# Performance work log

Hardware: AMD Instinct MI355X
Metric: run time of the kernel (lower is better)

Reference implementation:

```python
import jax, jax.numpy as jnp
import numpy as np

DN = ('NCHW', 'OIHW', 'NCHW')
EPS = 1e-5


def _mask_time(x, lengths):
    # zero out positions t >= length along the last (time) axis
    T = x.shape[-1]
    valid = jnp.arange(T)[None, None, None, :] < lengths[:, None, None, None]
    return jnp.where(valid, x, jnp.zeros((), x.dtype))


def _conv(x, w, b, stride, pad):
    y = jax.lax.conv_general_dilated(x, w, window_strides=stride,
                                     padding=[(pad[0], pad[0]), (pad[1], pad[1])],
                                     dimension_numbers=DN)
    return y + b[None, :, None, None]


def _bn(x, g, be, m, v):
    inv = jax.lax.rsqrt(v + EPS)
    return (x - m[None, :, None, None]) * (g * inv)[None, :, None, None] + be[None, :, None, None]


def setup_inputs() -> dict:
    key = jax.random.key(0)
    ks = jax.random.split(key, 16)
    f32 = jnp.float32
    return {
        'x': jax.random.normal(ks[0], (16, 1, 161, 1024), f32),
        'x_lengths': jax.random.randint(ks[1], (16,), 1, 512),
        'w1': jax.random.normal(ks[2], (32, 1, 41, 11), f32) * 0.05,
        'b1': jax.random.normal(ks[3], (32,), f32) * 0.05,
        'g1': jax.random.uniform(ks[4], (32,), f32) + 0.5,
        'be1': jax.random.normal(ks[5], (32,), f32) * 0.05,
        'm1': jax.random.normal(ks[6], (32,), f32) * 0.05,
        'v1': jax.random.uniform(ks[7], (32,), f32) + 0.5,
        'w2': jax.random.normal(ks[8], (32, 32, 21, 11), f32) * 0.02,
        'b2': jax.random.normal(ks[9], (32,), f32) * 0.05,
        'g2': jax.random.uniform(ks[10], (32,), f32) + 0.5,
        'be2': jax.random.normal(ks[11], (32,), f32) * 0.05,
        'm2': jax.random.normal(ks[12], (32,), f32) * 0.05,
        'v2': jax.random.uniform(ks[13], (32,), f32) + 0.5,
    }


def reference(x, x_lengths, w1, b1, g1, be1, m1, v1, w2, b2, g2, be2, m2, v2):
    # module 1: conv1 -> mask
    h = _mask_time(_conv(x, w1, b1, (2, 2), (20, 5)), x_lengths)   # [16,32,81,512]
    # module 2: bn1 -> mask
    h = _mask_time(_bn(h, g1, be1, m1, v1), x_lengths)
    # module 3: hardtanh(0,20) -> mask
    h = _mask_time(jnp.clip(h, 0.0, 20.0), x_lengths)
    # module 4: conv2 -> mask
    h = _mask_time(_conv(h, w2, b2, (2, 1), (10, 5)), x_lengths)   # [16,32,41,512]
    # module 5: bn2 -> mask
    h = _mask_time(_bn(h, g2, be2, m2, v2), x_lengths)
    # module 6: hardtanh(0,20) -> mask
    h = _mask_time(jnp.clip(h, 0.0, 20.0), x_lengths)
    return h
```

## Files before the change

### kernel.cpp

```cpp
#include <hip/hip_runtime.h>

typedef __attribute__((ext_vector_type(8))) __bf16 bf16x8;
typedef __attribute__((ext_vector_type(16))) float f32x16;

__device__ __forceinline__ unsigned short f2bf(float f) {
    unsigned int u = __float_as_uint(f);
    unsigned int r = (u + 0x7FFFu + ((u >> 16) & 1u)) >> 16;
    return (unsigned short)r;
}

#define GLL16(gp, lp) \
    __builtin_amdgcn_global_load_lds( \
        (const __attribute__((address_space(1))) unsigned int*)(gp), \
        (__attribute__((address_space(3))) unsigned int*)(lp), 16, 0, 0)

__global__ __launch_bounds__(256) void prep_w1t(const float* __restrict__ w1,
                                                unsigned short* __restrict__ w1t)
{
    const int t = blockIdx.x * 256 + threadIdx.x;
    const int k    = t % 48;
    const int rest = t / 48;
    const int oc   = rest & 31;
    const int kw   = rest >> 5;
    unsigned short v = 0;
    if (k < 41) v = f2bf(w1[(oc * 41 + k) * 11 + kw]);
    w1t[t] = v;
}

__global__ __launch_bounds__(256) void prep_w2f(const float* __restrict__ w2,
                                                unsigned short* __restrict__ w2tf)
{
    const int gid = blockIdx.x * 256 + threadIdx.x;
    const int j  = gid & 7;
    const int l  = (gid >> 3) & 63;
    const int s  = (gid >> 9) & 1;
    const int ti = gid >> 10;
    const int khpp = ti / 11;
    const int kw   = ti - khpp * 11;
    const int kh   = khpp - 4;
    const int oc   = l & 31;
    const int ic   = s * 16 + ((l >> 5) << 3) + j;
    unsigned short v = 0;
    if ((unsigned)kh <= 20u)
        v = f2bf(w2[((oc * 32 + ic) * 21 + kh) * 11 + kw]);
    w2tf[gid] = v;
}

__global__ __launch_bounds__(256) void zero_halo(unsigned short* __restrict__ h1s)
{
    const int id = blockIdx.x * 256 + threadIdx.x;
    if (id >= 51840) return;
    const int k  = id % 10;
    const int qq = (id / 10) & 3;
    const int nr = id / 40;
    const int c  = (k < 5) ? 11 + k : 523 + k;
    uint4 z = {0u, 0u, 0u, 0u};
    *(uint4*)((char*)h1s + ((size_t)(nr * 4 + qq) * 544 + c) * 16) = z;
}

__global__ __launch_bounds__(256) void conv1_mfma(
    const float* __restrict__ x, const int* __restrict__ xlen,
    const unsigned short* __restrict__ w1t,
    const float* __restrict__ b1, const float* __restrict__ g1,
    const float* __restrict__ be1, const float* __restrict__ m1,
    const float* __restrict__ v1,
    unsigned short* __restrict__ h1s)
{
    __shared__ uint4 lds4[2128];
    char* lds = (char*)lds4;

    const int t  = threadIdx.x;
    const int bx = blockIdx.x;
    const int yi = blockIdx.y;
    const int n  = blockIdx.z;
    const int oh0 = ((yi >> 2) << 3) + (yi & 3);
    const int len = xlen[n];

    const int l   = t & 63;
    const int w   = t >> 6;
    const int l31 = l & 31;
    const int lhi = l >> 5;

    char* h8 = (char*)h1s;
    const size_t rowpitch = 34816;

    if (bx * 128 >= len) {
        #pragma unroll
        for (int it = 0; it < 4; ++it) {
            const int idx = t + it * 256;
            const int d1 = idx >> 9;
            const int q  = (idx >> 7) & 3;
            const int cl = idx & 127;
            const int oh = oh0 + 4 * d1;
            if (oh <= 80) {
                uint4 z = {0u, 0u, 0u, 0u};
                *(uint4*)(h8 + (size_t)(n * 81 + oh) * rowpitch + q * 8704
                          + (16 + (bx << 7) + cl) * 16) = z;
            }
        }
        return;
    }

    const int cw   = t & 63;
    const int jrow = t >> 6;
    const int gr0  = 2 * oh0 - 20;
    const int gc0  = bx * 256 - 5;
    const float* xn = x + (size_t)n * 161 * 1024;
    #pragma unroll
    for (int cg = 0; cg < 5; ++cg) {
        const int c = cg * 64 + cw;
        if (c < 266) {
            const int gc = gc0 + c;
            const bool cok = (gc >= 0) && (gc < 1024);
            #pragma unroll
            for (int jj = 0; jj < 2; ++jj) {
                const int j = jrow + 4 * jj;
                if (j < 7) {
                    unsigned int u[4];
                    #pragma unroll
                    for (int q = 0; q < 4; ++q) {
                        const int rA = gr0 + 8 * j + 2 * q;
                        float lo = 0.f, hi = 0.f;
                        if (cok && rA >= 0 && rA < 161)         lo = xn[(size_t)rA * 1024 + gc];
                        if (cok && rA + 1 >= 0 && rA + 1 < 161) hi = xn[(size_t)(rA + 1) * 1024 + gc];
                        u[q] = (unsigned int)f2bf(lo) | ((unsigned int)f2bf(hi) << 16);
                    }
                    uint4 val; val.x = u[0]; val.y = u[1]; val.z = u[2]; val.w = u[3];
                    *(uint4*)(lds + c * 128 + ((j ^ ((c >> 1) & 7)) << 4)) = val;
                }
            }
        }
    }
    __syncthreads();

    const int i = (w << 5) + l31;

    f32x16 acc0 = {}, acc1 = {};
    const char* w1tb = (const char*)w1t;
    #pragma unroll
    for (int kw = 0; kw < 11; ++kw) {
        const char* ap = w1tb + kw * 3072 + l31 * 96 + lhi * 16;
        const bf16x8 a0 = *(const bf16x8*)(ap);
        const bf16x8 a1 = *(const bf16x8*)(ap + 32);
        const bf16x8 a2 = *(const bf16x8*)(ap + 64);
        const int c = 2 * i + kw;
        const char* cb = lds + c * 128;
        const int sw = (c >> 1) & 7;
        const bf16x8 b00 = *(const bf16x8*)(cb + (((0 + lhi) ^ sw) << 4));
        const bf16x8 b01 = *(const bf16x8*)(cb + (((2 + lhi) ^ sw) << 4));
        const bf16x8 b02 = *(const bf16x8*)(cb + (((4 + lhi) ^ sw) << 4));
        const bf16x8 b10 = *(const bf16x8*)(cb + (((1 + lhi) ^ sw) << 4));
        const bf16x8 b11 = *(const bf16x8*)(cb + (((3 + lhi) ^ sw) << 4));
        const bf16x8 b12 = *(const bf16x8*)(cb + (((5 + lhi) ^ sw) << 4));
        acc0 = __builtin_amdgcn_mfma_f32_32x32x16_bf16(a0, b00, acc0, 0, 0, 0);
        acc0 = __builtin_amdgcn_mfma_f32_32x32x16_bf16(a1, b01, acc0, 0, 0, 0);
        acc0 = __builtin_amdgcn_mfma_f32_32x32x16_bf16(a2, b02, acc0, 0, 0, 0);
        acc1 = __builtin_amdgcn_mfma_f32_32x32x16_bf16(a0, b10, acc1, 0, 0, 0);
        acc1 = __builtin_amdgcn_mfma_f32_32x32x16_bf16(a1, b11, acc1, 0, 0, 0);
        acc1 = __builtin_amdgcn_mfma_f32_32x32x16_bf16(a2, b12, acc1, 0, 0, 0);
    }

    __syncthreads();
    const int ow  = bx * 128 + i;
    const bool vmask = ow < len;
    #pragma unroll
    for (int d1 = 0; d1 < 2; ++d1) {
        const int oh = oh0 + 4 * d1;
        if (oh <= 80) {
            #pragma unroll
            for (int q = 0; q < 4; ++q) {
                float vv[4];
                #pragma unroll
                for (int rr = 0; rr < 4; ++rr) {
                    const int reg = (q << 2) + rr;
                    const int oc  = rr + (q << 3) + (lhi << 2);
                    const float s = g1[oc] * rsqrtf(v1[oc] + 1e-5f);
                    float val = ((d1 ? acc1[reg] : acc0[reg]) + b1[oc] - m1[oc]) * s + be1[oc];
                    val = fminf(fmaxf(val, 0.f), 20.f);
                    vv[rr] = vmask ? val : 0.f;
                }
                uint2 pk;
                pk.x = (unsigned int)f2bf(vv[0]) | ((unsigned int)f2bf(vv[1]) << 16);
                pk.y = (unsigned int)f2bf(vv[2]) | ((unsigned int)f2bf(vv[3]) << 16);
                *(uint2*)(lds + (((d1 << 2) + q) << 11) + i * 16 + lhi * 8) = pk;
            }
        }
    }
    __syncthreads();
    #pragma unroll
    for (int it = 0; it < 4; ++it) {
        const int idx = t + it * 256;
        const int d1 = idx >> 9;
        const int q  = (idx >> 7) & 3;
        const int cl = idx & 127;
        const int oh = oh0 + 4 * d1;
        if (oh <= 80) {
            const uint4 v = *(const uint4*)(lds + (((d1 << 2) + q) << 11) + cl * 16);
            *(uint4*)(h8 + (size_t)(n * 81 + oh) * rowpitch + q * 8704
                      + (16 + (bx << 7) + cl) * 16) = v;
        }
    }
}

__global__ __launch_bounds__(128, 2) void conv2_v12(
    const unsigned short* __restrict__ h1s, const unsigned short* __restrict__ w2tf,
    const int* __restrict__ xlen,
    const float* __restrict__ b2, const float* __restrict__ g2,
    const float* __restrict__ be2, const float* __restrict__ m2,
    const float* __restrict__ v2, float* __restrict__ out)
{
    __shared__ char ring[3 * 6144];

    const int t   = threadIdx.x;
    const int w   = t >> 6;
    const int l   = t & 63;
    const int l31 = l & 31;
    const int lhi = l >> 5;

    const int bid = blockIdx.x;
    const int lb  = (bid & 7) * 336 + (bid >> 3);
    const int n   = lb / 168;
    const int rem = lb - n * 168;
    const int by  = rem >> 3;
    const int bx  = rem & 7;

    const int ow0 = bx << 6;
    const int len = xlen[n];
    const int by4 = by << 2;

    if (ow0 >= len) {
        const int oh2 = 2 * by + w;
        if (oh2 <= 40) {
            #pragma unroll
            for (int f = 0; f < 2; ++f) {
                const int ow = ow0 + (f << 5) + l31;
                #pragma unroll
                for (int reg = 0; reg < 16; ++reg) {
                    const int oc = (reg & 3) + ((reg >> 2) << 3) + (lhi << 2);
                    out[((size_t)(n * 32 + oc) * 41 + oh2) * 512 + ow] = 0.f;
                }
            }
        }
        return;
    }

    const int rlo = (by4 - 10 > 0) ? by4 - 10 : 0;
    const int rhi = (by4 + 12 < 80) ? by4 + 12 : 80;

    f32x16 a00 = {}, a01 = {}, a10 = {}, a11 = {};

    const char* nb2 = (const char*)h1s + (size_t)(n * 81) * 34816;
    const char* w8v = (const char*)w2tf;

    int gso[3], lso[3];
    #pragma unroll
    for (int i = 0; i < 3; ++i) {
        const int idx = w * 192 + i * 64 + l;
        const int q   = idx / 96;
        const int c   = idx - q * 96;
        gso[i] = q * 8704 + (ow0 + 11 + c) * 16;
        lso[i] = idx * 16;
    }

    #define STAGE(r, buf) do { \
        const char* g_ = nb2 + (size_t)(r) * 34816; \
        char* d_ = ring + (buf) * 6144; \
        GLL16(g_ + gso[0], d_ + lso[0]); \
        GLL16(g_ + gso[1], d_ + lso[1]); \
        GLL16(g_ + gso[2], d_ + lso[2]); \
    } while (0)

    #define LOADB(S, ibv) do { \
        _Pragma("unroll") \
        for (int kw = 0; kw < 11; ++kw) \
            S[kw] = *(const bf16x8*)(w8v \
                + (size_t)((((ibv) * 11 + kw) * 2 + w) << 10) + (l << 4)); \
    } while (0)

    #define MFMAS(AJ0, AJ1, bufi) do { \
        const char* lb8_ = ring + (bufi) * 6144 + ((2 * w + lhi) * 96) * 16; \
        _Pragma("unroll") \
        for (int kw = 0; kw < 11; ++kw) { \
            const bf16x8 B0 = *(const bf16x8*)(lb8_ + (l31 + kw) * 16); \
            const bf16x8 B1 = *(const bf16x8*)(lb8_ + (l31 + kw + 32) * 16); \
            a00 = __builtin_amdgcn_mfma_f32_32x32x16_bf16(AJ0[kw], B0, a00, 0, 0, 0); \
            a01 = __builtin_amdgcn_mfma_f32_32x32x16_bf16(AJ0[kw], B1, a01, 0, 0, 0); \
            a10 = __builtin_amdgcn_mfma_f32_32x32x16_bf16(AJ1[kw], B0, a10, 0, 0, 0); \
            a11 = __builtin_amdgcn_mfma_f32_32x32x16_bf16(AJ1[kw], B1, a11, 0, 0, 0); \
        } \
    } while (0)

    #define ITER(kk, SC, SP, stbuf, rdbuf) do { \
        const int r_ = rlo + (kk); \
        LOADB(SC, r_ - by4 + 14); \
        { const int rs_ = (r_ + 2 <= rhi) ? (r_ + 2) : rhi; STAGE(rs_, stbuf); } \
        asm volatile("s_waitcnt vmcnt(3)" ::: "memory"); \
        __builtin_amdgcn_sched_barrier(0); \
        MFMAS(SC, SP, rdbuf); \
    } while (0)

    bf16x8 S0[11], S1[11], S2[11];
    LOADB(S1, rlo - by4 + 12);
    LOADB(S2, rlo - by4 + 13);
    STAGE(rlo,     0);
    STAGE(rlo + 1, 1);

    const int trips = rhi - rlo + 1;
    int k = 0;
    for (; k + 3 <= trips; k += 3) {
        ITER(k,     S0, S1, 2, 0);
        ITER(k + 1, S1, S2, 0, 1);
        ITER(k + 2, S2, S0, 1, 2);
    }
    if (k < trips)     { ITER(k,     S0, S1, 2, 0); }
    if (k + 1 < trips) { ITER(k + 1, S1, S2, 0, 1); }
    #undef ITER
    #undef MFMAS
    #undef LOADB
    #undef STAGE

    __syncthreads();
    if (w == 1) {
        #define WRPART(ACC, fi) do { \
            char* dst_ = ring + (fi) * 4096 + l * 64; \
            _Pragma("unroll") \
            for (int q = 0; q < 4; ++q) { \
                float4 v_; \
                v_.x = ACC[4*q]; v_.y = ACC[4*q+1]; v_.z = ACC[4*q+2]; v_.w = ACC[4*q+3]; \
                *(float4*)(dst_ + q * 16) = v_; \
            } \
        } while (0)
        WRPART(a00, 0); WRPART(a01, 1); WRPART(a10, 2); WRPART(a11, 3);
        #undef WRPART
    }
    __syncthreads();
    if (w == 1) return;

    #define STOUT(ACC, fi, jv, fv) do { \
        const int oh2_ = 2 * by + (jv); \
        if (oh2_ <= 40) { \
            const char* src_ = ring + (fi) * 4096 + l * 64; \
            float pr_[16]; \
            _Pragma("unroll") \
            for (int q = 0; q < 4; ++q) { \
                const float4 v_ = *(const float4*)(src_ + q * 16); \
                pr_[4*q] = v_.x; pr_[4*q+1] = v_.y; pr_[4*q+2] = v_.z; pr_[4*q+3] = v_.w; \
            } \
            const int ow_ = ow0 + ((fv) << 5) + l31; \
            const bool valid_ = ow_ < len; \
            _Pragma("unroll") \
            for (int reg = 0; reg < 16; ++reg) { \
                const int oc_ = (reg & 3) + ((reg >> 2) << 3) + (lhi << 2); \
                const float sc_ = g2[oc_] * rsqrtf(v2[oc_] + 1e-5f); \
                float val_ = (ACC[reg] + pr_[reg] + b2[oc_] - m2[oc_]) * sc_ + be2[oc_]; \
                val_ = fminf(fmaxf(val_, 0.f), 20.f); \
                if (!valid_) val_ = 0.f; \
                out[((size_t)(n * 32 + oc_) * 41 + oh2_) * 512 + ow_] = val_; \
            } \
        } \
    } while (0)
    STOUT(a00, 0, 0, 0); STOUT(a01, 1, 0, 1); STOUT(a10, 2, 1, 0); STOUT(a11, 3, 1, 1);
    #undef STOUT
}

extern "C" void kernel_launch(void* const* d_in, const int* in_sizes, int n_in,
                              void* d_out, int out_size, void* d_ws, size_t ws_size,
                              hipStream_t stream) {
    const float* x    = (const float*)d_in[0];
    const int*   xlen = (const int*)  d_in[1];
    const float* w1   = (const float*)d_in[2];
    const float* b1   = (const float*)d_in[3];
    const float* g1   = (const float*)d_in[4];
    const float* be1  = (const float*)d_in[5];
    const float* m1   = (const float*)d_in[6];
    const float* v1   = (const float*)d_in[7];
    const float* w2   = (const float*)d_in[8];
    const float* b2   = (const float*)d_in[9];
    const float* g2   = (const float*)d_in[10];
    const float* be2  = (const float*)d_in[11];
    const float* m2   = (const float*)d_in[12];
    const float* v2   = (const float*)d_in[13];
    float* out = (float*)d_out;

    unsigned short* h1s  = (unsigned short*)d_ws;
    unsigned short* w2tf = h1s + 22560768;
    unsigned short* w1t  = w2tf + 349184;

    prep_w1t<<<dim3(66),   dim3(256), 0, stream>>>(w1, w1t);
    prep_w2f<<<dim3(1364), dim3(256), 0, stream>>>(w2, w2tf);
    zero_halo<<<dim3(203), dim3(256), 0, stream>>>(h1s);
    conv1_mfma<<<dim3(4, 41, 16), dim3(256), 0, stream>>>(
        x, xlen, w1t, b1, g1, be1, m1, v1, h1s);
    conv2_v12<<<dim3(2688), dim3(128), 0, stream>>>(
        h1s, w2tf, xlen, b2, g2, be2, m2, v2, out);
}
```

Baseline: 193.3 us.

## Widen conv2 output tile to 96 columns with three MFMA column fragments

```diff
diff --git a/kernel.cpp b/kernel.cpp
--- a/kernel.cpp
+++ b/kernel.cpp
@@ -202,14 +202,14 @@
     }
 }
 
-__global__ __launch_bounds__(128, 2) void conv2_v12(
+__global__ __launch_bounds__(128, 2) void conv2_v14(
     const unsigned short* __restrict__ h1s, const unsigned short* __restrict__ w2tf,
     const int* __restrict__ xlen,
     const float* __restrict__ b2, const float* __restrict__ g2,
     const float* __restrict__ be2, const float* __restrict__ m2,
     const float* __restrict__ v2, float* __restrict__ out)
 {
-    __shared__ char ring[3 * 6144];
+    __shared__ char ring[3 * 8192];
 
     const int t   = threadIdx.x;
     const int w   = t >> 6;
@@ -218,13 +218,13 @@
     const int lhi = l >> 5;
 
     const int bid = blockIdx.x;
-    const int lb  = (bid & 7) * 336 + (bid >> 3);
-    const int n   = lb / 168;
-    const int rem = lb - n * 168;
-    const int by  = rem >> 3;
-    const int bx  = rem & 7;
-
-    const int ow0 = bx << 6;
+    const int lb  = (bid & 7) * 252 + (bid >> 3);
+    const int n   = lb / 126;
+    const int rem = lb - n * 126;
+    const int by  = rem / 6;
+    const int bx  = rem - by * 6;
+
+    const int ow0 = bx * 96;
     const int len = xlen[n];
     const int by4 = by << 2;
 
@@ -232,12 +232,14 @@
         const int oh2 = 2 * by + w;
         if (oh2 <= 40) {
             #pragma unroll
-            for (int f = 0; f < 2; ++f) {
+            for (int f = 0; f < 3; ++f) {
                 const int ow = ow0 + (f << 5) + l31;
-                #pragma unroll
-                for (int reg = 0; reg < 16; ++reg) {
-                    const int oc = (reg & 3) + ((reg >> 2) << 3) + (lhi << 2);
-                    out[((size_t)(n * 32 + oc) * 41 + oh2) * 512 + ow] = 0.f;
+                if (ow < 512) {
+                    #pragma unroll
+                    for (int reg = 0; reg < 16; ++reg) {
+                        const int oc = (reg & 3) + ((reg >> 2) << 3) + (lhi << 2);
+                        out[((size_t)(n * 32 + oc) * 41 + oh2) * 512 + ow] = 0.f;
+                    }
                 }
             }
         }
@@ -247,46 +249,50 @@
     const int rlo = (by4 - 10 > 0) ? by4 - 10 : 0;
     const int rhi = (by4 + 12 < 80) ? by4 + 12 : 80;
 
-    f32x16 a00 = {}, a01 = {}, a10 = {}, a11 = {};
+    f32x16 a00 = {}, a01 = {}, a02 = {};
+    f32x16 a10 = {}, a11 = {}, a12 = {};
 
     const char* nb2 = (const char*)h1s + (size_t)(n * 81) * 34816;
     const char* w8v = (const char*)w2tf;
 
-    int gso[3], lso[3];
+    int gso[4], lso[4];
     #pragma unroll
-    for (int i = 0; i < 3; ++i) {
-        const int idx = w * 192 + i * 64 + l;
-        const int q   = idx / 96;
-        const int c   = idx - q * 96;
+    for (int i = 0; i < 4; ++i) {
+        const int q = 2 * w + (i >> 1);
+        const int c = (i & 1) * 64 + l;
         gso[i] = q * 8704 + (ow0 + 11 + c) * 16;
-        lso[i] = idx * 16;
+        lso[i] = q * 2048 + c * 16;
     }
 
     #define STAGE(r, buf) do { \
         const char* g_ = nb2 + (size_t)(r) * 34816; \
-        char* d_ = ring + (buf) * 6144; \
+        char* d_ = ring + (buf) * 8192; \
         GLL16(g_ + gso[0], d_ + lso[0]); \
         GLL16(g_ + gso[1], d_ + lso[1]); \
         GLL16(g_ + gso[2], d_ + lso[2]); \
+        GLL16(g_ + gso[3], d_ + lso[3]); \
     } while (0)
 
-    #define LOADB(S, ibv) do { \
+    #define LOADB(S, khppv) do { \
         _Pragma("unroll") \
         for (int kw = 0; kw < 11; ++kw) \
             S[kw] = *(const bf16x8*)(w8v \
-                + (size_t)((((ibv) * 11 + kw) * 2 + w) << 10) + (l << 4)); \
+                + (size_t)((((khppv) * 11 + kw) * 2 + w) << 10) + (l << 4)); \
     } while (0)
 
-    #define MFMAS(AJ0, AJ1, bufi) do { \
-        const char* lb8_ = ring + (bufi) * 6144 + ((2 * w + lhi) * 96) * 16; \
+    #define MFMAS(SJ0, TJ1, bufi) do { \
+        const char* lb8_ = ring + (bufi) * 8192 + (2 * w + lhi) * 2048; \
         _Pragma("unroll") \
         for (int kw = 0; kw < 11; ++kw) { \
             const bf16x8 B0 = *(const bf16x8*)(lb8_ + (l31 + kw) * 16); \
             const bf16x8 B1 = *(const bf16x8*)(lb8_ + (l31 + kw + 32) * 16); \
-            a00 = __builtin_amdgcn_mfma_f32_32x32x16_bf16(AJ0[kw], B0, a00, 0, 0, 0); \
-            a01 = __builtin_amdgcn_mfma_f32_32x32x16_bf16(AJ0[kw], B1, a01, 0, 0, 0); \
-            a10 = __builtin_amdgcn_mfma_f32_32x32x16_bf16(AJ1[kw], B0, a10, 0, 0, 0); \
-            a11 = __builtin_amdgcn_mfma_f32_32x32x16_bf16(AJ1[kw], B1, a11, 0, 0, 0); \
+            const bf16x8 B2 = *(const bf16x8*)(lb8_ + (l31 + kw + 64) * 16); \
+            a00 = __builtin_amdgcn_mfma_f32_32x32x16_bf16(SJ0[kw], B0, a00, 0, 0, 0); \
+            a01 = __builtin_amdgcn_mfma_f32_32x32x16_bf16(SJ0[kw], B1, a01, 0, 0, 0); \
+            a02 = __builtin_amdgcn_mfma_f32_32x32x16_bf16(SJ0[kw], B2, a02, 0, 0, 0); \
+            a10 = __builtin_amdgcn_mfma_f32_32x32x16_bf16(TJ1[kw], B0, a10, 0, 0, 0); \
+            a11 = __builtin_amdgcn_mfma_f32_32x32x16_bf16(TJ1[kw], B1, a11, 0, 0, 0); \
+            a12 = __builtin_amdgcn_mfma_f32_32x32x16_bf16(TJ1[kw], B2, a12, 0, 0, 0); \
         } \
     } while (0)
 
@@ -294,7 +300,7 @@
         const int r_ = rlo + (kk); \
         LOADB(SC, r_ - by4 + 14); \
         { const int rs_ = (r_ + 2 <= rhi) ? (r_ + 2) : rhi; STAGE(rs_, stbuf); } \
-        asm volatile("s_waitcnt vmcnt(3)" ::: "memory"); \
+        asm volatile("s_waitcnt vmcnt(4)" ::: "memory"); \
         __builtin_amdgcn_sched_barrier(0); \
         MFMAS(SC, SP, rdbuf); \
     } while (0)
@@ -330,7 +336,8 @@
                 *(float4*)(dst_ + q * 16) = v_; \
             } \
         } while (0)
-        WRPART(a00, 0); WRPART(a01, 1); WRPART(a10, 2); WRPART(a11, 3);
+        WRPART(a00, 0); WRPART(a01, 1); WRPART(a02, 2);
+        WRPART(a10, 3); WRPART(a11, 4); WRPART(a12, 5);
         #undef WRPART
     }
     __syncthreads();
@@ -338,7 +345,8 @@
 
     #define STOUT(ACC, fi, jv, fv) do { \
         const int oh2_ = 2 * by + (jv); \
-        if (oh2_ <= 40) { \
+        const int ow_  = ow0 + ((fv) << 5) + l31; \
+        if (oh2_ <= 40 && ow_ < 512) { \
             const char* src_ = ring + (fi) * 4096 + l * 64; \
             float pr_[16]; \
             _Pragma("unroll") \
@@ -346,7 +354,6 @@
                 const float4 v_ = *(const float4*)(src_ + q * 16); \
                 pr_[4*q] = v_.x; pr_[4*q+1] = v_.y; pr_[4*q+2] = v_.z; pr_[4*q+3] = v_.w; \
             } \
-            const int ow_ = ow0 + ((fv) << 5) + l31; \
             const bool valid_ = ow_ < len; \
             _Pragma("unroll") \
             for (int reg = 0; reg < 16; ++reg) { \
@@ -359,7 +366,8 @@
             } \
         } \
     } while (0)
-    STOUT(a00, 0, 0, 0); STOUT(a01, 1, 0, 1); STOUT(a10, 2, 1, 0); STOUT(a11, 3, 1, 1);
+    STOUT(a00, 0, 0, 0); STOUT(a01, 1, 0, 1); STOUT(a02, 2, 0, 2);
+    STOUT(a10, 3, 1, 0); STOUT(a11, 4, 1, 1); STOUT(a12, 5, 1, 2);
     #undef STOUT
 }
 
@@ -391,6 +399,6 @@
     zero_halo<<<dim3(203), dim3(256), 0, stream>>>(h1s);
     conv1_mfma<<<dim3(4, 41, 16), dim3(256), 0, stream>>>(
         x, xlen, w1t, b1, g1, be1, m1, v1, h1s);
-    conv2_v12<<<dim3(2688), dim3(128), 0, stream>>>(
+    conv2_v14<<<dim3(2016), dim3(128), 0, stream>>>(
         h1s, w2tf, xlen, b2, g2, be2, m2, v2, out);
 }
```

After: 213.6 us. 1.11x slower.
